# Performance work log

Measured on AMD Instinct MI355X. Metric: run time of the kernel, lower is better.

## Reference

```python
import jax, jax.numpy as jnp
import numpy as np

N, D_IN, HID, N_CLS, E = 100000, 256, 128, 41, 1600000


def setup_inputs() -> dict:
    key = jax.random.key(0)
    ks = jax.random.split(key, 8)
    x = jax.random.normal(ks[0], (N, D_IN), dtype=jnp.float32)
    edge_index = jax.random.randint(ks[1], (2, E), 0, N, dtype=jnp.int64)
    s = 1.0 / np.sqrt(D_IN)
    W1 = jax.random.uniform(ks[2], (D_IN, HID), jnp.float32, -s, s)
    b1 = jnp.zeros((HID,), jnp.float32)
    s2 = 1.0 / np.sqrt(HID)
    W2 = jax.random.uniform(ks[3], (HID, HID), jnp.float32, -s2, s2)
    b2 = jnp.zeros((HID,), jnp.float32)
    lin_w = jax.random.uniform(ks[4], (HID, N_CLS), jnp.float32, -s2, s2)
    lin_b = jnp.zeros((N_CLS,), jnp.float32)
    return {"x": x, "edge_index": edge_index, "W1": W1, "b1": b1,
            "W2": W2, "b2": b2, "lin_w": lin_w, "lin_b": lin_b}


def _gcn_conv(h, src, dst, norm, W, b, n):
    # h: [N, F_in]; transform then gather-scale-scatter (PyG GCNConv order)
    h = h @ W                                   # [N, F_out]
    msg = h[src] * norm[:, None]                # [E+N, F_out]
    return jax.ops.segment_sum(msg, dst, num_segments=n) + b


def reference(x, edge_index, W1, b1, W2, b2, lin_w, lin_b):
    n = x.shape[0]
    loops = jnp.arange(n, dtype=edge_index.dtype)
    src = jnp.concatenate([edge_index[0], loops])  # add self-loops
    dst = jnp.concatenate([edge_index[1], loops])
    # symmetric normalization D^-1/2 (A+I) D^-1/2
    deg = jax.ops.segment_sum(jnp.ones_like(dst, dtype=x.dtype), dst, num_segments=n)
    dis = jnp.where(deg > 0, jax.lax.rsqrt(jnp.maximum(deg, 1.0)), 0.0)
    norm = dis[src] * dis[dst]                   # [E+N]

    x1 = jax.nn.relu(_gcn_conv(x, src, dst, norm, W1, b1, n))   # dropout is identity in eval
    x2 = jax.nn.relu(_gcn_conv(x1, src, dst, norm, W2, b2, n))
    out = (x1 + x2) @ lin_w + lin_b
    return jax.nn.log_softmax(out, axis=1)
```

## Files before the change

kernel.cpp:

```cpp
#include <hip/hip_runtime.h>
#include <math.h>


#define NPAD (1 << 17)
#define CHUNK 1024

typedef __attribute__((ext_vector_type(8))) short short8;
typedef __attribute__((ext_vector_type(4))) float f32x4;

__device__ inline unsigned short f2bf(float f) {
    unsigned u = __builtin_bit_cast(unsigned, f);
    return (unsigned short)((u + 0x7fffu + ((u >> 16) & 1u)) >> 16);
}
__device__ inline float bflo(unsigned u) { return __builtin_bit_cast(float, u << 16); }
__device__ inline float bfhi(unsigned u) { return __builtin_bit_cast(float, u & 0xffff0000u); }


__global__ void hist_kernel(const int* __restrict__ dst, int* __restrict__ cnt, int E) {
    int e = blockIdx.x * 256 + threadIdx.x;
    if (e < E) atomicAdd(&cnt[dst[e]], 1);
}

__global__ void scan_partial(const int* __restrict__ cnt, int* __restrict__ partial, int n) {
    __shared__ int sdata[4];
    int b = blockIdx.x, t = threadIdx.x;
    int base = b * CHUNK;
    int sum = 0;
    for (int i = t; i < CHUNK; i += 256) {
        int idx = base + i;
        if (idx < n) sum += cnt[idx];
    }
#pragma unroll
    for (int off = 32; off > 0; off >>= 1) sum += __shfl_down(sum, off, 64);
    if ((t & 63) == 0) sdata[t >> 6] = sum;
    __syncthreads();
    if (t == 0) partial[b] = sdata[0] + sdata[1] + sdata[2] + sdata[3];
}

__global__ void scan_small(int* partial, int nblk) {
    __shared__ int sm[128];
    int t = threadIdx.x;
    int v = (t < nblk) ? partial[t] : 0;
    int x = v;
    sm[t] = x;
    __syncthreads();
    for (int off = 1; off < 128; off <<= 1) {
        int y = (t >= off) ? sm[t - off] : 0;
        __syncthreads();
        x += y;
        sm[t] = x;
        __syncthreads();
    }
    if (t < nblk) partial[t] = x - v;
}

__global__ void scan_final(const int* __restrict__ cnt, const int* __restrict__ partial,
                           int* __restrict__ offs, int* __restrict__ cursor,
                           float* __restrict__ dis, int n) {
    __shared__ int wsum[4];
    int b = blockIdx.x, t = threadIdx.x;
    int lane = t & 63, w = t >> 6;
    int base = b * CHUNK + t * 4;
    int v[4];
#pragma unroll
    for (int j = 0; j < 4; j++) v[j] = (base + j < n) ? cnt[base + j] : 0;
    int s4 = v[0] + v[1] + v[2] + v[3];
    int inc = s4;
#pragma unroll
    for (int off = 1; off < 64; off <<= 1) {
        int x = __shfl_up(inc, off, 64);
        if (lane >= off) inc += x;
    }
    if (lane == 63) wsum[w] = inc;
    __syncthreads();
    int woff = 0;
    for (int i = 0; i < 4; i++) if (i < w) woff += wsum[i];
    int pos = partial[b] + woff + (inc - s4);
#pragma unroll
    for (int j = 0; j < 4; j++) {
        int idx = base + j;
        if (idx < n) {
            offs[idx] = pos;
            cursor[idx] = pos;
            dis[idx] = rsqrtf((float)(v[j] + 1));
            pos += v[j];
        }
    }
}

__global__ void permute_all(const int* __restrict__ src, const int* __restrict__ dst,
                            const float* __restrict__ dis,
                            int* __restrict__ cursor, int2* __restrict__ eadj, int E) {
    int e = blockIdx.x * 256 + threadIdx.x;
    if (e < E) {
        int d = dst[e];
        int s = src[e];
        int pos = atomicAdd(&cursor[d], 1);
        float wt = dis[s] * dis[d];
        eadj[pos] = make_int2(s, __float_as_int(wt));
    }
}

__global__ void wcast2(const float* __restrict__ W1, unsigned short* __restrict__ Wt1,
                       const float* __restrict__ W2, unsigned short* __restrict__ Wt2) {
    int i = blockIdx.x * 256 + threadIdx.x;
    if (i < 256 * 128) {
        int k = i >> 7, nn = i & 127;
        Wt1[nn * 256 + k] = f2bf(W1[i]);
    } else {
        int j = i - 256 * 128;
        if (j < 128 * 128) {
            int k = j >> 7, nn = j & 127;
            Wt2[nn * 128 + k] = f2bf(W2[j]);
        }
    }
}

template<bool ABF16>
__global__ __launch_bounds__(256) void gemm_mfma(const void* __restrict__ Ap,
                                                 const unsigned short* __restrict__ Wt,
                                                 unsigned short* __restrict__ Hb,
                                                 int n, int K) {
    __shared__ unsigned short bs[128 * 136];
    const int tid = threadIdx.x;
    const int wave = tid >> 6, lane = tid & 63;
    const int quad = lane >> 4, mrow = lane & 15;
    const int arow_g = blockIdx.x * 64 + wave * 16 + mrow;
    const int arow = arow_g < n ? arow_g : n - 1;

    f32x4 acc[8];
#pragma unroll
    for (int t = 0; t < 8; t++) acc[t] = (f32x4){0.f, 0.f, 0.f, 0.f};

    const float* Af = (const float*)Ap;
    const unsigned short* Ab = (const unsigned short*)Ap;

    for (int kc = 0; kc < K; kc += 128) {
        __syncthreads();
        for (int i = tid; i < 2048; i += 256) {
            int row = i >> 4, c8 = i & 15;
            *(short8*)&bs[row * 136 + c8 * 8] = *(const short8*)&Wt[row * K + kc + c8 * 8];
        }
        __syncthreads();
#pragma unroll
        for (int kt = 0; kt < 128; kt += 32) {
            union { short8 v; unsigned short u[8]; } A;
            if (ABF16) {
                A.v = *(const short8*)&Ab[(size_t)arow * K + kc + kt + quad * 8];
            } else {
                const float* ap = &Af[(size_t)arow * K + kc + kt + quad * 8];
                float4 p0 = *(const float4*)ap;
                float4 p1 = *(const float4*)(ap + 4);
                A.u[0] = f2bf(p0.x); A.u[1] = f2bf(p0.y);
                A.u[2] = f2bf(p0.z); A.u[3] = f2bf(p0.w);
                A.u[4] = f2bf(p1.x); A.u[5] = f2bf(p1.y);
                A.u[6] = f2bf(p1.z); A.u[7] = f2bf(p1.w);
            }
#pragma unroll
            for (int nt = 0; nt < 8; nt++) {
                short8 B = *(const short8*)&bs[(nt * 16 + mrow) * 136 + kt + quad * 8];
                acc[nt] = __builtin_amdgcn_mfma_f32_16x16x32_bf16(A.v, B, acc[nt], 0, 0, 0);
            }
        }
    }
    const int drow0 = blockIdx.x * 64 + wave * 16 + quad * 4;
#pragma unroll
    for (int r = 0; r < 4; r++) {
        int dr = drow0 + r;
        if (dr < n) {
#pragma unroll
            for (int nt = 0; nt < 8; nt++)
                Hb[(size_t)dr * 128 + nt * 16 + mrow] = f2bf(acc[nt][r]);
        }
    }
}

template<bool FUSE>
__global__ __launch_bounds__(256) void gather_k(const unsigned short* __restrict__ Hb,
                                                const int2* __restrict__ eadj,
                                                const int* __restrict__ offs,
                                                const int* __restrict__ cnt,
                                                const float* __restrict__ dis,
                                                const float* __restrict__ bias,
                                                unsigned short* __restrict__ outb,
                                                const unsigned short* __restrict__ x1b,
                                                const float* __restrict__ lw,
                                                const float* __restrict__ lb,
                                                float* __restrict__ out, int n) {
    __shared__ float s[4][128];
    const int w = threadIdx.x >> 6, lane = threadIdx.x & 63;
    const int grp = lane >> 4, fl = lane & 15;
    const int node = blockIdx.x * 4 + w;
    const int nd = node < n ? node : n - 1;
    const int st = offs[nd], c = cnt[nd];
    const unsigned short* Hfl = Hb + fl * 8;

    float acc[8];
#pragma unroll
    for (int k = 0; k < 8; k++) acc[k] = 0.f;

    const int2* ep = eadj + st;
    for (int kk = 0; kk < c; kk += 64) {
        int li = kk + lane;
        int2 me = ep[li < c ? li : c - 1];
        float mw = li < c ? __int_as_float(me.y) : 0.f;
        int cend = (c - kk) < 64 ? (c - kk) : 64;

        int   s0 = __shfl(me.x, grp, 64);
        float w0 = __shfl(mw,  grp, 64);
        int   s1 = __shfl(me.x, 4 + grp, 64);
        float w1 = __shfl(mw,  4 + grp, 64);
        uint4 r0 = *(const uint4*)(Hfl + (size_t)s0 * 128);
        uint4 r1 = *(const uint4*)(Hfl + (size_t)s1 * 128);

        for (int j = 0; j < cend; j += 8) {
            int jn = (j + 8 < cend) ? j + 8 : j;
            int   sn0 = __shfl(me.x, jn + grp, 64);
            float wn0 = __shfl(mw,  jn + grp, 64);
            int   sn1 = __shfl(me.x, jn + 4 + grp, 64);
            float wn1 = __shfl(mw,  jn + 4 + grp, 64);
            uint4 rn0 = *(const uint4*)(Hfl + (size_t)sn0 * 128);
            uint4 rn1 = *(const uint4*)(Hfl + (size_t)sn1 * 128);
            acc[0] = fmaf(bflo(r0.x), w0, acc[0]); acc[1] = fmaf(bfhi(r0.x), w0, acc[1]);
            acc[2] = fmaf(bflo(r0.y), w0, acc[2]); acc[3] = fmaf(bfhi(r0.y), w0, acc[3]);
            acc[4] = fmaf(bflo(r0.z), w0, acc[4]); acc[5] = fmaf(bfhi(r0.z), w0, acc[5]);
            acc[6] = fmaf(bflo(r0.w), w0, acc[6]); acc[7] = fmaf(bfhi(r0.w), w0, acc[7]);
            acc[0] = fmaf(bflo(r1.x), w1, acc[0]); acc[1] = fmaf(bfhi(r1.x), w1, acc[1]);
            acc[2] = fmaf(bflo(r1.y), w1, acc[2]); acc[3] = fmaf(bfhi(r1.y), w1, acc[3]);
            acc[4] = fmaf(bflo(r1.z), w1, acc[4]); acc[5] = fmaf(bfhi(r1.z), w1, acc[5]);
            acc[6] = fmaf(bflo(r1.w), w1, acc[6]); acc[7] = fmaf(bfhi(r1.w), w1, acc[7]);
            r0 = rn0; r1 = rn1; w0 = wn0; w1 = wn1;
        }
    }
#pragma unroll
    for (int k = 0; k < 8; k++) {
        acc[k] += __shfl_xor(acc[k], 16, 64);
        acc[k] += __shfl_xor(acc[k], 32, 64);
    }
    float dd = dis[nd], sn = dd * dd;
    uint4 rs = *(const uint4*)(Hfl + (size_t)nd * 128);
    float4 bb0 = ((const float4*)bias)[fl * 2];
    float4 bb1 = ((const float4*)bias)[fl * 2 + 1];
    acc[0] = fmaf(bflo(rs.x), sn, acc[0]) + bb0.x;
    acc[1] = fmaf(bfhi(rs.x), sn, acc[1]) + bb0.y;
    acc[2] = fmaf(bflo(rs.y), sn, acc[2]) + bb0.z;
    acc[3] = fmaf(bfhi(rs.y), sn, acc[3]) + bb0.w;
    acc[4] = fmaf(bflo(rs.z), sn, acc[4]) + bb1.x;
    acc[5] = fmaf(bfhi(rs.z), sn, acc[5]) + bb1.y;
    acc[6] = fmaf(bflo(rs.w), sn, acc[6]) + bb1.z;
    acc[7] = fmaf(bfhi(rs.w), sn, acc[7]) + bb1.w;
#pragma unroll
    for (int k = 0; k < 8; k++) acc[k] = acc[k] > 0.f ? acc[k] : 0.f;

    if (!FUSE) {
        if (node < n && grp == 0) {
            uint4 pk;
            pk.x = ((unsigned)f2bf(acc[1]) << 16) | (unsigned)f2bf(acc[0]);
            pk.y = ((unsigned)f2bf(acc[3]) << 16) | (unsigned)f2bf(acc[2]);
            pk.z = ((unsigned)f2bf(acc[5]) << 16) | (unsigned)f2bf(acc[4]);
            pk.w = ((unsigned)f2bf(acc[7]) << 16) | (unsigned)f2bf(acc[6]);
            *(uint4*)(outb + (size_t)node * 128 + fl * 8) = pk;
        }
    } else {
        if (grp == 0) {
            uint4 xv = *(const uint4*)(x1b + (size_t)nd * 128 + fl * 8);
            s[w][fl * 8 + 0] = acc[0] + bflo(xv.x);
            s[w][fl * 8 + 1] = acc[1] + bfhi(xv.x);
            s[w][fl * 8 + 2] = acc[2] + bflo(xv.y);
            s[w][fl * 8 + 3] = acc[3] + bfhi(xv.y);
            s[w][fl * 8 + 4] = acc[4] + bflo(xv.z);
            s[w][fl * 8 + 5] = acc[5] + bfhi(xv.z);
            s[w][fl * 8 + 6] = acc[6] + bflo(xv.w);
            s[w][fl * 8 + 7] = acc[7] + bfhi(xv.w);
        }
        __syncthreads();
        bool act = (node < n) && (lane < 41);
        float val = 0.f;
        if (act) {
#pragma unroll 4
            for (int f = 0; f < 128; f++) val = fmaf(s[w][f], lw[f * 41 + lane], val);
            val += lb[lane];
        }
        float m = act ? val : -INFINITY;
#pragma unroll
        for (int off = 32; off > 0; off >>= 1) m = fmaxf(m, __shfl_xor(m, off, 64));
        float e = act ? expf(val - m) : 0.f;
#pragma unroll
        for (int off = 32; off > 0; off >>= 1) e += __shfl_xor(e, off, 64);
        if (act) out[(size_t)node * 41 + lane] = val - m - logf(e);
    }
}

extern "C" void kernel_launch(void* const* d_in, const int* in_sizes, int n_in,
                              void* d_out, int out_size, void* d_ws, size_t ws_size,
                              hipStream_t stream) {
    const float* x  = (const float*)d_in[0];
    const int*   ei = (const int*)d_in[1];
    const float* W1 = (const float*)d_in[2];
    const float* b1 = (const float*)d_in[3];
    const float* W2 = (const float*)d_in[4];
    const float* b2 = (const float*)d_in[5];
    const float* lw = (const float*)d_in[6];
    const float* lb = (const float*)d_in[7];
    float* out = (float*)d_out;

    const int n = in_sizes[0] / 256;
    const int E = in_sizes[1] / 2;
    const int* src = ei;
    const int* dst = ei + E;

    int*   cnt     = (int*)d_ws;
    int*   offs    = cnt + NPAD;
    int*   cursor  = offs + NPAD;
    int*   partial = cursor + NPAD;
    float* dis     = (float*)(partial + 1024);
    size_t Epad    = ((size_t)E + 255) & ~(size_t)255;
    int2*  eadj    = (int2*)(dis + NPAD);
    unsigned short* Wt1 = (unsigned short*)(eadj + Epad);
    unsigned short* Wt2 = Wt1 + 256 * 128;
    unsigned short* Hb  = Wt2 + 128 * 128;
    unsigned short* X1b = Hb + (size_t)n * 128;

    const int nscan = (n + CHUNK - 1) / CHUNK;

    hipMemsetAsync(cnt, 0, (size_t)n * sizeof(int), stream);
    wcast2<<<(256 * 128 + 128 * 128 + 255) / 256, 256, 0, stream>>>(W1, Wt1, W2, Wt2);

    hist_kernel<<<(E + 255) / 256, 256, 0, stream>>>(dst, cnt, E);
    scan_partial<<<nscan, 256, 0, stream>>>(cnt, partial, n);
    scan_small<<<1, 128, 0, stream>>>(partial, nscan);
    scan_final<<<nscan, 256, 0, stream>>>(cnt, partial, offs, cursor, dis, n);
    permute_all<<<(E + 255) / 256, 256, 0, stream>>>(src, dst, dis, cursor, eadj, E);

    gemm_mfma<false><<<(n + 63) / 64, 256, 0, stream>>>(x, Wt1, Hb, n, 256);
    gather_k<false><<<(n + 3) / 4, 256, 0, stream>>>(Hb, eadj, offs, cnt, dis, b1, X1b,
                                                     nullptr, nullptr, nullptr, nullptr, n);

    gemm_mfma<true><<<(n + 63) / 64, 256, 0, stream>>>(X1b, Wt2, Hb, n, 128);
    gather_k<true><<<(n + 3) / 4, 256, 0, stream>>>(Hb, eadj, offs, cnt, dis, b2, nullptr,
                                                    X1b, lw, lb, out, n);
}
```

Baseline: 587.5 us.

## Merge independent launches and split gather feature halves across XCD-mapped blocks

Merges the weight cast into the histogram kernel and the edge permutation into the first GEMM launch, so independent work shares one grid and launch gaps shrink. The gather kernel now has each block handle half of the 128 features, with block indices remapped so paired halves of the same nodes land on the same XCD group, aiming for better L2 locality of the gathered rows. The classifier head moves into its own kernel that reads bf16 X1 and X2, which costs an extra launch and an extra round trip of X2 through memory. It also doubles the number of gather blocks, so edge lists are read twice.

Result: slower. 616.1 us (+4.9%).

```diff
diff --git a/kernel.cpp b/kernel.cpp
--- a/kernel.cpp
+++ b/kernel.cpp
@@ -16,9 +16,26 @@
 __device__ inline float bfhi(unsigned u) { return __builtin_bit_cast(float, u & 0xffff0000u); }
 
 
-__global__ void hist_kernel(const int* __restrict__ dst, int* __restrict__ cnt, int E) {
-    int e = blockIdx.x * 256 + threadIdx.x;
-    if (e < E) atomicAdd(&cnt[dst[e]], 1);
+__global__ void mega1(const int* __restrict__ dst, int* __restrict__ cnt, int E, int histB,
+                      const float* __restrict__ W1, unsigned short* __restrict__ Wt1,
+                      const float* __restrict__ W2, unsigned short* __restrict__ Wt2) {
+    int b = blockIdx.x;
+    if (b < histB) {
+        int e = b * 256 + threadIdx.x;
+        if (e < E) atomicAdd(&cnt[dst[e]], 1);
+    } else {
+        int i = (b - histB) * 256 + threadIdx.x;
+        if (i < 256 * 128) {
+            int k = i >> 7, nn = i & 127;
+            Wt1[nn * 256 + k] = f2bf(W1[i]);
+        } else {
+            int j = i - 256 * 128;
+            if (j < 128 * 128) {
+                int k = j >> 7, nn = j & 127;
+                Wt2[nn * 128 + k] = f2bf(W2[j]);
+            }
+        }
+    }
 }
 
 __global__ void scan_partial(const int* __restrict__ cnt, int* __restrict__ partial, int n) {
@@ -88,44 +105,15 @@
     }
 }
 
-__global__ void permute_all(const int* __restrict__ src, const int* __restrict__ dst,
-                            const float* __restrict__ dis,
-                            int* __restrict__ cursor, int2* __restrict__ eadj, int E) {
-    int e = blockIdx.x * 256 + threadIdx.x;
-    if (e < E) {
-        int d = dst[e];
-        int s = src[e];
-        int pos = atomicAdd(&cursor[d], 1);
-        float wt = dis[s] * dis[d];
-        eadj[pos] = make_int2(s, __float_as_int(wt));
-    }
-}
-
-__global__ void wcast2(const float* __restrict__ W1, unsigned short* __restrict__ Wt1,
-                       const float* __restrict__ W2, unsigned short* __restrict__ Wt2) {
-    int i = blockIdx.x * 256 + threadIdx.x;
-    if (i < 256 * 128) {
-        int k = i >> 7, nn = i & 127;
-        Wt1[nn * 256 + k] = f2bf(W1[i]);
-    } else {
-        int j = i - 256 * 128;
-        if (j < 128 * 128) {
-            int k = j >> 7, nn = j & 127;
-            Wt2[nn * 128 + k] = f2bf(W2[j]);
-        }
-    }
-}
-
 template<bool ABF16>
-__global__ __launch_bounds__(256) void gemm_mfma(const void* __restrict__ Ap,
-                                                 const unsigned short* __restrict__ Wt,
-                                                 unsigned short* __restrict__ Hb,
-                                                 int n, int K) {
-    __shared__ unsigned short bs[128 * 136];
+__device__ void gemm_body(int bid, const void* __restrict__ Ap,
+                          const unsigned short* __restrict__ Wt,
+                          unsigned short* __restrict__ Hb,
+                          int n, int K, unsigned short* bs) {
     const int tid = threadIdx.x;
     const int wave = tid >> 6, lane = tid & 63;
     const int quad = lane >> 4, mrow = lane & 15;
-    const int arow_g = blockIdx.x * 64 + wave * 16 + mrow;
+    const int arow_g = bid * 64 + wave * 16 + mrow;
     const int arow = arow_g < n ? arow_g : n - 1;
 
     f32x4 acc[8];
@@ -163,7 +151,7 @@
             }
         }
     }
-    const int drow0 = blockIdx.x * 64 + wave * 16 + quad * 4;
+    const int drow0 = bid * 64 + wave * 16 + quad * 4;
 #pragma unroll
     for (int r = 0; r < 4; r++) {
         int dr = drow0 + r;
@@ -175,25 +163,54 @@
     }
 }
 
-template<bool FUSE>
-__global__ __launch_bounds__(256) void gather_k(const unsigned short* __restrict__ Hb,
+__global__ __launch_bounds__(256) void mega2(const int* __restrict__ src,
+                                             const int* __restrict__ dst,
+                                             const float* __restrict__ dis,
+                                             int* __restrict__ cursor,
+                                             int2* __restrict__ eadj, int E, int permB,
+                                             const float* __restrict__ x,
+                                             const unsigned short* __restrict__ Wt1,
+                                             unsigned short* __restrict__ Hb, int n) {
+    __shared__ unsigned short bs[128 * 136];
+    int b = blockIdx.x;
+    if (b < permB) {
+        int e = b * 256 + threadIdx.x;
+        if (e < E) {
+            int d = dst[e];
+            int s = src[e];
+            int pos = atomicAdd(&cursor[d], 1);
+            eadj[pos] = make_int2(s, __float_as_int(dis[s] * dis[d]));
+        }
+    } else {
+        gemm_body<false>(b - permB, x, Wt1, Hb, n, 256, bs);
+    }
+}
+
+__global__ __launch_bounds__(256) void gemm2_k(const unsigned short* __restrict__ X1b,
+                                               const unsigned short* __restrict__ Wt2,
+                                               unsigned short* __restrict__ Hb, int n) {
+    __shared__ unsigned short bs[128 * 136];
+    gemm_body<true>(blockIdx.x, X1b, Wt2, Hb, n, 128, bs);
+}
+
+__global__ __launch_bounds__(256) void gather_h(const unsigned short* __restrict__ Hb,
                                                 const int2* __restrict__ eadj,
                                                 const int* __restrict__ offs,
                                                 const int* __restrict__ cnt,
                                                 const float* __restrict__ dis,
                                                 const float* __restrict__ bias,
                                                 unsigned short* __restrict__ outb,
-                                                const unsigned short* __restrict__ x1b,
-                                                const float* __restrict__ lw,
-                                                const float* __restrict__ lb,
-                                                float* __restrict__ out, int n) {
-    __shared__ float s[4][128];
+                                                int n) {
+    const int b = blockIdx.x;
+    const int xcd = b & 7;
+    const int half = xcd >> 2;
+    const int nb = ((b >> 3) << 2) | (xcd & 3);
     const int w = threadIdx.x >> 6, lane = threadIdx.x & 63;
-    const int grp = lane >> 4, fl = lane & 15;
-    const int node = blockIdx.x * 4 + w;
+    const int grp = lane >> 3, fl = lane & 7;
+    const int node = nb * 4 + w;
     const int nd = node < n ? node : n - 1;
     const int st = offs[nd], c = cnt[nd];
-    const unsigned short* Hfl = Hb + fl * 8;
+    const unsigned short* Hfl = Hb + half * 64 + fl * 8;
 
     float acc[8];
 #pragma unroll
@@ -208,17 +225,17 @@
 
         int   s0 = __shfl(me.x, grp, 64);
         float w0 = __shfl(mw,  grp, 64);
-        int   s1 = __shfl(me.x, 4 + grp, 64);
-        float w1 = __shfl(mw,  4 + grp, 64);
+        int   s1 = __shfl(me.x, 8 + grp, 64);
+        float w1 = __shfl(mw,  8 + grp, 64);
         uint4 r0 = *(const uint4*)(Hfl + (size_t)s0 * 128);
         uint4 r1 = *(const uint4*)(Hfl + (size_t)s1 * 128);
 
-        for (int j = 0; j < cend; j += 8) {
-            int jn = (j + 8 < cend) ? j + 8 : j;
+        for (int j = 0; j < cend; j += 16) {
+            int jn = (j + 16 < cend) ? j + 16 : j;
             int   sn0 = __shfl(me.x, jn + grp, 64);
             float wn0 = __shfl(mw,  jn + grp, 64);
-            int   sn1 = __shfl(me.x, jn + 4 + grp, 64);
-            float wn1 = __shfl(mw,  jn + 4 + grp, 64);
+            int   sn1 = __shfl(me.x, jn + 8 + grp, 64);
+            float wn1 = __shfl(mw,  jn + 8 + grp, 64);
             uint4 rn0 = *(const uint4*)(Hfl + (size_t)sn0 * 128);
             uint4 rn1 = *(const uint4*)(Hfl + (size_t)sn1 * 128);
             acc[0] = fmaf(bflo(r0.x), w0, acc[0]); acc[1] = fmaf(bfhi(r0.x), w0, acc[1]);
@@ -234,13 +251,14 @@
     }
 #pragma unroll
     for (int k = 0; k < 8; k++) {
+        acc[k] += __shfl_xor(acc[k], 8, 64);
         acc[k] += __shfl_xor(acc[k], 16, 64);
         acc[k] += __shfl_xor(acc[k], 32, 64);
     }
     float dd = dis[nd], sn = dd * dd;
     uint4 rs = *(const uint4*)(Hfl + (size_t)nd * 128);
-    float4 bb0 = ((const float4*)bias)[fl * 2];
-    float4 bb1 = ((const float4*)bias)[fl * 2 + 1];
+    float4 bb0 = ((const float4*)bias)[half * 16 + fl * 2];
+    float4 bb1 = ((const float4*)bias)[half * 16 + fl * 2 + 1];
     acc[0] = fmaf(bflo(rs.x), sn, acc[0]) + bb0.x;
     acc[1] = fmaf(bfhi(rs.x), sn, acc[1]) + bb0.y;
     acc[2] = fmaf(bflo(rs.y), sn, acc[2]) + bb0.z;
@@ -252,43 +270,43 @@
 #pragma unroll
     for (int k = 0; k < 8; k++) acc[k] = acc[k] > 0.f ? acc[k] : 0.f;
 
-    if (!FUSE) {
-        if (node < n && grp == 0) {
-            uint4 pk;
-            pk.x = ((unsigned)f2bf(acc[1]) << 16) | (unsigned)f2bf(acc[0]);
-            pk.y = ((unsigned)f2bf(acc[3]) << 16) | (unsigned)f2bf(acc[2]);
-            pk.z = ((unsigned)f2bf(acc[5]) << 16) | (unsigned)f2bf(acc[4]);
-            pk.w = ((unsigned)f2bf(acc[7]) << 16) | (unsigned)f2bf(acc[6]);
-            *(uint4*)(outb + (size_t)node * 128 + fl * 8) = pk;
-        }
-    } else {
-        if (grp == 0) {
-            uint4 xv = *(const uint4*)(x1b + (size_t)nd * 128 + fl * 8);
-            s[w][fl * 8 + 0] = acc[0] + bflo(xv.x);
-            s[w][fl * 8 + 1] = acc[1] + bfhi(xv.x);
-            s[w][fl * 8 + 2] = acc[2] + bflo(xv.y);
-            s[w][fl * 8 + 3] = acc[3] + bfhi(xv.y);
-            s[w][fl * 8 + 4] = acc[4] + bflo(xv.z);
-            s[w][fl * 8 + 5] = acc[5] + bfhi(xv.z);
-            s[w][fl * 8 + 6] = acc[6] + bflo(xv.w);
-            s[w][fl * 8 + 7] = acc[7] + bfhi(xv.w);
-        }
-        __syncthreads();
-        bool act = (node < n) && (lane < 41);
-        float val = 0.f;
-        if (act) {
+    if (node < n && grp == 0) {
+        uint4 pk;
+        pk.x = ((unsigned)f2bf(acc[1]) << 16) | (unsigned)f2bf(acc[0]);
+        pk.y = ((unsigned)f2bf(acc[3]) << 16) | (unsigned)f2bf(acc[2]);
+        pk.z = ((unsigned)f2bf(acc[5]) << 16) | (unsigned)f2bf(acc[4]);
+        pk.w = ((unsigned)f2bf(acc[7]) << 16) | (unsigned)f2bf(acc[6]);
+        *(uint4*)(outb + (size_t)node * 128 + half * 64 + fl * 8) = pk;
+    }
+}
+
+__global__ __launch_bounds__(256) void head_k(const unsigned short* __restrict__ x1b,
+                                              const unsigned short* __restrict__ x2b,
+                                              const float* __restrict__ lw,
+                                              const float* __restrict__ lb,
+                                              float* __restrict__ out, int n) {
+    __shared__ float s[4][128];
+    const int w = threadIdx.x >> 6, lane = threadIdx.x & 63;
+    const int node = blockIdx.x * 4 + w;
+    const int nd = node < n ? node : n - 1;
+    unsigned u1 = *(const unsigned*)(x1b + (size_t)nd * 128 + lane * 2);
+    unsigned u2 = *(const unsigned*)(x2b + (size_t)nd * 128 + lane * 2);
+    s[w][lane * 2]     = bflo(u1) + bflo(u2);
+    s[w][lane * 2 + 1] = bfhi(u1) + bfhi(u2);
+    bool act = (node < n) && (lane < 41);
+    float val = 0.f;
+    if (act) {
 #pragma unroll 4
-            for (int f = 0; f < 128; f++) val = fmaf(s[w][f], lw[f * 41 + lane], val);
-            val += lb[lane];
-        }
-        float m = act ? val : -INFINITY;
-#pragma unroll
-        for (int off = 32; off > 0; off >>= 1) m = fmaxf(m, __shfl_xor(m, off, 64));
-        float e = act ? expf(val - m) : 0.f;
-#pragma unroll
-        for (int off = 32; off > 0; off >>= 1) e += __shfl_xor(e, off, 64);
-        if (act) out[(size_t)node * 41 + lane] = val - m - logf(e);
-    }
+        for (int f = 0; f < 128; f++) val = fmaf(s[w][f], lw[f * 41 + lane], val);
+        val += lb[lane];
+    }
+    float m = act ? val : -INFINITY;
+#pragma unroll
+    for (int off = 32; off > 0; off >>= 1) m = fmaxf(m, __shfl_xor(m, off, 64));
+    float e = act ? expf(val - m) : 0.f;
+#pragma unroll
+    for (int off = 32; off > 0; off >>= 1) e += __shfl_xor(e, off, 64);
+    if (act) out[(size_t)node * 41 + lane] = val - m - logf(e);
 }
 
 extern "C" void kernel_launch(void* const* d_in, const int* in_sizes, int n_in,
@@ -320,23 +338,30 @@
     unsigned short* Wt2 = Wt1 + 256 * 128;
     unsigned short* Hb  = Wt2 + 128 * 128;
     unsigned short* X1b = Hb + (size_t)n * 128;
+    unsigned short* X2b = X1b + (size_t)n * 128;
 
     const int nscan = (n + CHUNK - 1) / CHUNK;
+    const int histB = (E + 255) / 256;
+    const int wcastB = (256 * 128 + 128 * 128 + 255) / 256;
+    const int permB = histB;
+    const int gemmB = (n + 63) / 64;
+    const int NB = (n + 3) / 4;
+    const int gathB = 8 * ((NB + 3) / 4);
 
     hipMemsetAsync(cnt, 0, (size_t)n * sizeof(int), stream);
-    wcast2<<<(256 * 128 + 128 * 128 + 255) / 256, 256, 0, stream>>>(W1, Wt1, W2, Wt2);
-
-    hist_kernel<<<(E + 255) / 256, 256, 0, stream>>>(dst, cnt, E);
+
+    mega1<<<histB + wcastB, 256, 0, stream>>>(dst, cnt, E, histB, W1, Wt1, W2, Wt2);
     scan_partial<<<nscan, 256, 0, stream>>>(cnt, partial, n);
     scan_small<<<1, 128, 0, stream>>>(partial, nscan);
     scan_final<<<nscan, 256, 0, stream>>>(cnt, partial, offs, cursor, dis, n);
-    permute_all<<<(E + 255) / 256, 256, 0, stream>>>(src, dst, dis, cursor, eadj, E);
-
-    gemm_mfma<false><<<(n + 63) / 64, 256, 0, stream>>>(x, Wt1, Hb, n, 256);
-    gather_k<false><<<(n + 3) / 4, 256, 0, stream>>>(Hb, eadj, offs, cnt, dis, b1, X1b,
-                                                     nullptr, nullptr, nullptr, nullptr, n);
-
-    gemm_mfma<true><<<(n + 63) / 64, 256, 0, stream>>>(X1b, Wt2, Hb, n, 128);
-    gather_k<true><<<(n + 3) / 4, 256, 0, stream>>>(Hb, eadj, offs, cnt, dis, b2, nullptr,
-                                                    X1b, lw, lb, out, n);
-}
+
+    mega2<<<permB + gemmB, 256, 0, stream>>>(src, dst, dis, cursor, eadj, E, permB,
+                                             x, Wt1, Hb, n);
+
+    gather_h<<<gathB, 256, 0, stream>>>(Hb, eadj, offs, cnt, dis, b1, X1b, n);
+
+    gemm2_k<<<gemmB, 256, 0, stream>>>(X1b, Wt2, Hb, n);
+    gather_h<<<gathB, 256, 0, stream>>>(Hb, eadj, offs, cnt, dis, b2, X2b, n);
+
+    head_k<<<NB, 256, 0, stream>>>(X1b, X2b, lw, lb, out, n);
+}
```
